# Kernel optimization log

Hardware: AMD Instinct MI355X
Metric: run time of the kernel (lower is better)

## Reference

```python
import jax, jax.numpy as jnp
import numpy as np

C = 512
NUM_HEADS = 8
HEAD_DIM = C // NUM_HEADS


def setup_inputs() -> dict:
    key = jax.random.key(0)
    ks = jax.random.split(key, 9)
    s = 1.0 / np.sqrt(C)
    x = jax.random.normal(ks[0], (8, C, 32, 32), dtype=jnp.float32)
    Wq = jax.random.uniform(ks[1], (C, C), jnp.float32, -s, s)
    bq = jax.random.uniform(ks[2], (C,), jnp.float32, -s, s)
    Wk = jax.random.uniform(ks[3], (C, C), jnp.float32, -s, s)
    bk = jax.random.uniform(ks[4], (C,), jnp.float32, -s, s)
    Wv = jax.random.uniform(ks[5], (C, C), jnp.float32, -s, s)
    bv = jax.random.uniform(ks[6], (C,), jnp.float32, -s, s)
    Wo = jax.random.uniform(ks[7], (C, C), jnp.float32, -s, s)
    bo = jax.random.uniform(ks[8], (C,), jnp.float32, -s, s)
    return {"x": x, "Wq": Wq, "bq": bq, "Wk": Wk, "bk": bk,
            "Wv": Wv, "bv": bv, "Wo": Wo, "bo": bo}


def reference(x, Wq, bq, Wk, bk, Wv, bv, Wo, bo):
    N, Cc, H, W = x.shape
    S = H * W
    # [N, S, C] token sequence
    xs = x.reshape(N, Cc, S).transpose(0, 2, 1)
    # torch Linear: y = x @ W^T + b
    q = xs @ Wq.T + bq
    k = xs @ Wk.T + bk
    v = xs @ Wv.T + bv
    # [N, h, S, d]
    q = q.reshape(N, S, NUM_HEADS, HEAD_DIM).transpose(0, 2, 1, 3)
    k = k.reshape(N, S, NUM_HEADS, HEAD_DIM).transpose(0, 2, 1, 3)
    v = v.reshape(N, S, NUM_HEADS, HEAD_DIM).transpose(0, 2, 1, 3)
    energy = jnp.einsum('nhqd,nhkd->nhqk', q, k)
    attn = jax.nn.softmax(energy / np.sqrt(HEAD_DIM), axis=3)
    out = jnp.einsum('nhql,nhld->nhqd', attn, v)
    # back to [N, S, C]; note torch reshape from (N,h,S,d) order
    out = out.reshape(N, Cc, S) if False else out.reshape(N, -1, Cc)
    out = out @ Wo.T + bo
    return out.reshape(N, Cc, H, W)


if __name__ == "__main__":
    o = reference(**setup_inputs())
    print(o.shape)
```

## Files before the change

### kernel.cpp

```cpp
#include <hip/hip_runtime.h>


typedef _Float16 f16x8 __attribute__((ext_vector_type(8)));
typedef _Float16 f16x4 __attribute__((ext_vector_type(4)));
typedef float f32x4 __attribute__((ext_vector_type(4)));

__device__ inline void gl_lds16(const void* g, void* l) {
  __builtin_amdgcn_global_load_lds((const __attribute__((address_space(1))) void*)g,
                                   (__attribute__((address_space(3))) void*)l, 16, 0, 0);
}

__device__ inline float fexp2(float x) {
#if __has_builtin(__builtin_amdgcn_exp2f)
  return __builtin_amdgcn_exp2f(x);
#else
  return exp2f(x);
#endif
}

__global__ void prep(const float* __restrict__ x,
                     const float* __restrict__ Wq, const float* __restrict__ bq,
                     const float* __restrict__ Wk, const float* __restrict__ bk,
                     const float* __restrict__ Wv, const float* __restrict__ bv,
                     const float* __restrict__ Wo,
                     _Float16* __restrict__ xs16, _Float16* __restrict__ Wqkv16,
                     float* __restrict__ bqkv, _Float16* __restrict__ Wo16) {
  __shared__ float t[32][33];
  const int tid = threadIdx.x;
  if (blockIdx.x < 1024) {
    const float g = 0.18033688011112042f;
    int i = blockIdx.x * 256 + tid;
    Wqkv16[i]          = (_Float16)(Wq[i] * g);
    Wqkv16[262144 + i] = (_Float16)Wk[i];
    Wqkv16[524288 + i] = (_Float16)Wv[i];
    Wo16[i]            = (_Float16)Wo[i];
    if (i < 512) {
      bqkv[i]        = bq[i] * g;
      bqkv[512 + i]  = bk[i];
      bqkv[1024 + i] = bv[i];
    }
    return;
  }
  const int bid = blockIdx.x - 1024;
  const int n = bid >> 9, c0 = ((bid >> 5) & 15) * 32, s0 = (bid & 31) * 32;
  const int tx = tid & 31, ty = tid >> 5;
#pragma unroll
  for (int i = 0; i < 4; ++i) {
    int cc = ty + i * 8;
    t[cc][tx] = x[((size_t)n * 512 + c0 + cc) * 1024 + s0 + tx];
  }
  __syncthreads();
#pragma unroll
  for (int i = 0; i < 4; ++i) {
    int ss = ty + i * 8;
    xs16[((size_t)n * 1024 + s0 + ss) * 512 + c0 + tx] = (_Float16)t[tx][ss];
  }
}

__global__ __launch_bounds__(256, 2) void qkv_gemm(
    const _Float16* __restrict__ A, const _Float16* __restrict__ Bw,
    const float* __restrict__ bias, _Float16* __restrict__ QK,
    _Float16* __restrict__ Vt) {
  __shared__ _Float16 smem[16896];
  _Float16* As = smem;
  _Float16* Bs = smem + 8192;
  const int tid = threadIdx.x;
  const int lane = tid & 63, w = tid >> 6;
  const int quad = lane >> 4, l15 = lane & 15;
  const int bm = blockIdx.x * 128, bn = blockIdx.y * 128;
  const int wr = (w >> 1) * 64, wc = (w & 1) * 64;
  f32x4 acc[4][4] = {};
  for (int k0 = 0; k0 < 512; k0 += 64) {
    __syncthreads();
#pragma unroll
    for (int c = 0; c < 4; ++c) {
      int idx = c * 256 + tid;
      int row = idx >> 3, sc = idx & 7;
      int kg = sc ^ (row & 7);
      gl_lds16(A + (size_t)(bm + row) * 512 + k0 + kg * 8, As + idx * 8);
      gl_lds16(Bw + (size_t)(bn + row) * 512 + k0 + kg * 8, Bs + idx * 8);
    }
    __syncthreads();
#pragma unroll
    for (int kh = 0; kh < 2; ++kh) {
      f16x8 af[4], bf[4];
#pragma unroll
      for (int i = 0; i < 4; ++i) {
        int ra = wr + i * 16 + l15;
        af[i] = *(const f16x8*)(As + ra * 64 + ((kh * 4 + quad) ^ (ra & 7)) * 8);
        int rb = wc + i * 16 + l15;
        bf[i] = *(const f16x8*)(Bs + rb * 64 + ((kh * 4 + quad) ^ (rb & 7)) * 8);
      }
#pragma unroll
      for (int i = 0; i < 4; ++i)
#pragma unroll
        for (int j = 0; j < 4; ++j)
          acc[i][j] = __builtin_amdgcn_mfma_f32_16x16x32_f16(af[i], bf[j], acc[i][j], 0, 0, 0);
    }
  }
  if (blockIdx.y < 8) {
#pragma unroll
    for (int j = 0; j < 4; ++j) {
      int col = bn + wc + j * 16 + l15;
      float bb = bias[col];
#pragma unroll
      for (int i = 0; i < 4; ++i) {
        int rowb = bm + wr + i * 16 + quad * 4;
#pragma unroll
        for (int r = 0; r < 4; ++r)
          QK[(size_t)(rowb + r) * 1024 + col] = (_Float16)(acc[i][j][r] + bb);
      }
    }
  } else {
    __syncthreads();
#pragma unroll
    for (int j = 0; j < 4; ++j) {
      int cl = wc + j * 16 + l15;
      float bb = bias[bn + cl];
#pragma unroll
      for (int i = 0; i < 4; ++i) {
        int row = wr + i * 16 + quad * 4;
        f16x4 pk;
#pragma unroll
        for (int r = 0; r < 4; ++r) pk[r] = (_Float16)(acc[i][j][r] + bb);
        *(f16x4*)(smem + cl * 132 + row) = pk;
      }
    }
    __syncthreads();
    const int n = bm >> 10, s0g = bm & 1023;
    const int vh = (bn - 1024) >> 6;
    const int cl = tid >> 1, par = tid & 1;
    const int hh = vh + (cl >> 6), d = cl & 63;
    const size_t vrow = (((size_t)((n * 8 + hh) * 64 + d)) << 10) + s0g;
#pragma unroll
    for (int g = 0; g < 8; ++g) {
      int pb = g * 16 + par * 8;
      int a32 = pb & ~31, q = (pb >> 3) & 3;
      f16x4 lo = *(const f16x4*)(smem + cl * 132 + a32 + 4 * q);
      f16x4 hi = *(const f16x4*)(smem + cl * 132 + a32 + 16 + 4 * q);
      f16x8 o = {lo[0], lo[1], lo[2], lo[3], hi[0], hi[1], hi[2], hi[3]};
      *(f16x8*)(Vt + vrow + pb) = o;
    }
  }
}

__global__ __launch_bounds__(256, 2) void attn(
    const _Float16* __restrict__ QK, const _Float16* __restrict__ Vt,
    _Float16* __restrict__ O16) {
  __shared__ _Float16 Qs[128 * 64];
  __shared__ _Float16 Ks[128 * 64];
  __shared__ _Float16 Vs[64 * 128];
  const int tid = threadIdx.x, lane = tid & 63, w = tid >> 6;
  const int quad = lane >> 4, l15 = lane & 15;
  const int n = blockIdx.y >> 3, h = blockIdx.y & 7;
  const int q0 = blockIdx.x * 128;
#pragma unroll
  for (int c = 0; c < 4; ++c) {
    int idx = c * 256 + tid;
    int row = idx >> 3, sc = idx & 7;
    int dg = sc ^ (row & 7);
    gl_lds16(QK + (size_t)(n * 1024 + q0 + row) * 1024 + h * 64 + dg * 8, Qs + idx * 8);
  }
  __syncthreads();
  f16x8 qf[2][2];
#pragma unroll
  for (int mt = 0; mt < 2; ++mt)
#pragma unroll
    for (int dc = 0; dc < 2; ++dc) {
      int row = w * 32 + mt * 16 + l15;
      qf[mt][dc] = *(const f16x8*)(Qs + row * 64 + ((dc * 4 + quad) ^ (row & 7)) * 8);
    }
  f32x4 oaccT[4][2] = {};
  f32x4 lsum[2] = {};
  const f16x8 ones = {(_Float16)1, (_Float16)1, (_Float16)1, (_Float16)1,
                      (_Float16)1, (_Float16)1, (_Float16)1, (_Float16)1};

  for (int kt = 0; kt < 8; ++kt) {
    __syncthreads();
#pragma unroll
    for (int c = 0; c < 4; ++c) {
      int idx = c * 256 + tid;
      int row = idx >> 3, sck = idx & 7;
      int dg = sck ^ (row & 7);
      gl_lds16(QK + (size_t)(n * 1024 + kt * 128 + row) * 1024 + 512 + h * 64 + dg * 8,
               Ks + idx * 8);
      int d = idx >> 4, scv = idx & 15;
      int vg = scv ^ (d & 7);
      gl_lds16(Vt + (size_t)((n * 8 + h) * 64 + d) * 1024 + kt * 128 + vg * 8,
               Vs + idx * 8);
    }
    __syncthreads();
#pragma unroll
    for (int sc = 0; sc < 4; ++sc) {
      f32x4 sacc[2][2] = {};
#pragma unroll
      for (int t = 0; t < 2; ++t) {
        int rk = (sc * 2 + t) * 16 + l15;
        f16x8 kf0 = *(const f16x8*)(Ks + rk * 64 + ((quad) ^ (rk & 7)) * 8);
        f16x8 kf1 = *(const f16x8*)(Ks + rk * 64 + ((4 + quad) ^ (rk & 7)) * 8);
#pragma unroll
        for (int mt = 0; mt < 2; ++mt) {
          sacc[mt][t] = __builtin_amdgcn_mfma_f32_16x16x32_f16(kf0, qf[mt][0], sacc[mt][t], 0, 0, 0);
          sacc[mt][t] = __builtin_amdgcn_mfma_f32_16x16x32_f16(kf1, qf[mt][1], sacc[mt][t], 0, 0, 0);
        }
      }
      f16x8 pf[2];
#pragma unroll
      for (int mt = 0; mt < 2; ++mt) {
#pragma unroll
        for (int t = 0; t < 2; ++t)
#pragma unroll
          for (int r = 0; r < 4; ++r)
            pf[mt][t * 4 + r] = (_Float16)fexp2(sacc[mt][t][r]);
        lsum[mt] = __builtin_amdgcn_mfma_f32_16x16x32_f16(pf[mt], ones, lsum[mt], 0, 0, 0);
      }
#pragma unroll
      for (int nt = 0; nt < 4; ++nt) {
        int rd = nt * 16 + l15;
        f16x8 vf = *(const f16x8*)(Vs + rd * 128 + ((sc * 4 + quad) ^ (rd & 7)) * 8);
#pragma unroll
        for (int mt = 0; mt < 2; ++mt)
          oaccT[nt][mt] = __builtin_amdgcn_mfma_f32_16x16x32_f16(vf, pf[mt], oaccT[nt][mt], 0, 0, 0);
      }
    }
  }
#pragma unroll
  for (int mt = 0; mt < 2; ++mt) {
    int r3 = l15 & 3;
    float lv = lsum[mt][0];
    lv = (r3 == 1) ? lsum[mt][1] : lv;
    lv = (r3 == 2) ? lsum[mt][2] : lv;
    lv = (r3 == 3) ? lsum[mt][3] : lv;
    float lq = __shfl(lv, (l15 >> 2) * 16 + (l15 & 3), 64);
    float rinv = 1.0f / lq;
    int q = q0 + w * 32 + mt * 16 + l15;
    int i = h * 128 + (q >> 3);
    size_t base = (size_t)(n * 1024 + i) * 512 + (q & 7) * 64 + quad * 4;
#pragma unroll
    for (int nt = 0; nt < 4; ++nt) {
      f16x4 pk;
#pragma unroll
      for (int r = 0; r < 4; ++r) pk[r] = (_Float16)(oaccT[nt][mt][r] * rinv);
      *(f16x4*)(O16 + base + nt * 16) = pk;
    }
  }
}

__global__ __launch_bounds__(256, 2) void out_gemm(
    const _Float16* __restrict__ A, const _Float16* __restrict__ Bw,
    const float* __restrict__ bias, float* __restrict__ out) {
  __shared__ _Float16 As[128 * 32];
  __shared__ _Float16 Bs[128 * 32];
  const int tid = threadIdx.x;
  const int lane = tid & 63, w = tid >> 6;
  const int quad = lane >> 4, l15 = lane & 15;
  const int bm = blockIdx.x * 128, bn = blockIdx.y * 128;
  const int wr = (w >> 1) * 64, wc = (w & 1) * 64;
  f32x4 acc[4][4] = {};
  for (int k0 = 0; k0 < 512; k0 += 32) {
    __syncthreads();
#pragma unroll
    for (int c = 0; c < 2; ++c) {
      int idx = c * 256 + tid;
      int row = idx >> 2, sc = idx & 3;
      int kg = sc ^ ((row >> 1) & 3);
      gl_lds16(A + (size_t)(bm + row) * 512 + k0 + kg * 8, As + idx * 8);
      gl_lds16(Bw + (size_t)(bn + row) * 512 + k0 + kg * 8, Bs + idx * 8);
    }
    __syncthreads();
    f16x8 af[4], bf[4];
#pragma unroll
    for (int i = 0; i < 4; ++i) {
      int ra = wr + i * 16 + l15;
      af[i] = *(const f16x8*)(As + ra * 32 + (quad ^ ((ra >> 1) & 3)) * 8);
      int rb = wc + i * 16 + l15;
      bf[i] = *(const f16x8*)(Bs + rb * 32 + (quad ^ ((rb >> 1) & 3)) * 8);
    }
#pragma unroll
    for (int i = 0; i < 4; ++i)
#pragma unroll
      for (int j = 0; j < 4; ++j)
        acc[i][j] = __builtin_amdgcn_mfma_f32_16x16x32_f16(af[i], bf[j], acc[i][j], 0, 0, 0);
  }
#pragma unroll
  for (int j = 0; j < 4; ++j) {
    int col = bn + wc + j * 16 + l15;
    float bb = bias[col];
#pragma unroll
    for (int i = 0; i < 4; ++i) {
      int rowb = bm + wr + i * 16 + quad * 4;
#pragma unroll
      for (int r = 0; r < 4; ++r)
        out[(size_t)(rowb + r) * 512 + col] = acc[i][j][r] + bb;
    }
  }
}

extern "C" void kernel_launch(void* const* d_in, const int* in_sizes, int n_in,
                              void* d_out, int out_size, void* d_ws, size_t ws_size,
                              hipStream_t stream) {
  const float* x  = (const float*)d_in[0];
  const float* Wq = (const float*)d_in[1];
  const float* bq = (const float*)d_in[2];
  const float* Wk = (const float*)d_in[3];
  const float* bk = (const float*)d_in[4];
  const float* Wv = (const float*)d_in[5];
  const float* bv = (const float*)d_in[6];
  const float* Wo = (const float*)d_in[7];
  const float* bo = (const float*)d_in[8];
  float* out = (float*)d_out;
  char* ws = (char*)d_ws;

  _Float16* xs16   = (_Float16*)(ws);
  _Float16* QK     = (_Float16*)(ws + (8u << 20));
  _Float16* Vt     = (_Float16*)(ws + (24u << 20));
  _Float16* Wqkv16 = (_Float16*)(ws + (32u << 20));
  _Float16* Wo16   = (_Float16*)(ws + (32u << 20) + 1572864);
  float*    bqkv   = (float*)   (ws + (32u << 20) + 2097152);

  hipLaunchKernelGGL(prep, dim3(5120), dim3(256), 0, stream,
                     x, Wq, bq, Wk, bk, Wv, bv, Wo, xs16, Wqkv16, bqkv, Wo16);
  hipLaunchKernelGGL(qkv_gemm, dim3(64, 12), dim3(256), 0, stream,
                     xs16, Wqkv16, bqkv, QK, Vt);
  hipLaunchKernelGGL(attn, dim3(8, 64), dim3(256), 0, stream, QK, Vt, xs16);
  hipLaunchKernelGGL(out_gemm, dim3(64, 4), dim3(256), 0, stream,
                     xs16, Wo16, bo, out);
}
```

Before: 142.3 us.

## Fuse all four stages into one persistent kernel with grid barriers

Merges the prep, QKV GEMM, attention and output GEMM kernels into a single persistent kernel of 512 blocks, with atomic-counter grid barriers between stages. This removes three kernel launch boundaries and their drain and launch gaps, at the cost of a memset plus spin-wait barriers. It relies on all 512 blocks being co-resident (2 per CU via launch bounds); otherwise it could deadlock. Some stages now leave blocks idle, such as the output GEMM using only 256 blocks and the QKV GEMM looping over 768 tiles.

```diff
diff --git a/kernel.cpp b/kernel.cpp
--- a/kernel.cpp
+++ b/kernel.cpp
@@ -18,78 +18,274 @@
 #endif
 }
 
-__global__ void prep(const float* __restrict__ x,
-                     const float* __restrict__ Wq, const float* __restrict__ bq,
-                     const float* __restrict__ Wk, const float* __restrict__ bk,
-                     const float* __restrict__ Wv, const float* __restrict__ bv,
-                     const float* __restrict__ Wo,
-                     _Float16* __restrict__ xs16, _Float16* __restrict__ Wqkv16,
-                     float* __restrict__ bqkv, _Float16* __restrict__ Wo16) {
-  __shared__ float t[32][33];
+__device__ inline void gbar(unsigned* cnt, unsigned target) {
+  __syncthreads();
+  if (threadIdx.x == 0) {
+    __threadfence();
+    atomicAdd(cnt, 1u);
+    while (atomicAdd(cnt, 0u) < target) __builtin_amdgcn_s_sleep(8);
+    __threadfence();
+  }
+  __syncthreads();
+}
+
+__global__ __launch_bounds__(256, 2) void msa_fused(
+    const float* __restrict__ x,
+    const float* __restrict__ Wq, const float* __restrict__ bq,
+    const float* __restrict__ Wk, const float* __restrict__ bk,
+    const float* __restrict__ Wv, const float* __restrict__ bv,
+    const float* __restrict__ Wo, const float* __restrict__ bo,
+    float* __restrict__ out,
+    _Float16* __restrict__ xs16, _Float16* __restrict__ Wqkv16,
+    float* __restrict__ bqkv, _Float16* __restrict__ Wo16,
+    _Float16* __restrict__ QK, _Float16* __restrict__ Vt,
+    unsigned* __restrict__ bar) {
+  __shared__ __align__(16) char smem_raw[49152];
   const int tid = threadIdx.x;
-  if (blockIdx.x < 1024) {
+  const int bid = blockIdx.x;
+  const int lane = tid & 63, wv4 = tid >> 6;
+  const int quad = lane >> 4, l15 = lane & 15;
+
+  {
     const float g = 0.18033688011112042f;
-    int i = blockIdx.x * 256 + tid;
-    Wqkv16[i]          = (_Float16)(Wq[i] * g);
-    Wqkv16[262144 + i] = (_Float16)Wk[i];
-    Wqkv16[524288 + i] = (_Float16)Wv[i];
-    Wo16[i]            = (_Float16)Wo[i];
-    if (i < 512) {
-      bqkv[i]        = bq[i] * g;
-      bqkv[512 + i]  = bk[i];
-      bqkv[1024 + i] = bv[i];
-    }
-    return;
-  }
-  const int bid = blockIdx.x - 1024;
-  const int n = bid >> 9, c0 = ((bid >> 5) & 15) * 32, s0 = (bid & 31) * 32;
-  const int tx = tid & 31, ty = tid >> 5;
-#pragma unroll
-  for (int i = 0; i < 4; ++i) {
-    int cc = ty + i * 8;
-    t[cc][tx] = x[((size_t)n * 512 + c0 + cc) * 1024 + s0 + tx];
-  }
-  __syncthreads();
-#pragma unroll
-  for (int i = 0; i < 4; ++i) {
-    int ss = ty + i * 8;
-    xs16[((size_t)n * 1024 + s0 + ss) * 512 + c0 + tx] = (_Float16)t[tx][ss];
-  }
-}
-
-__global__ __launch_bounds__(256, 2) void qkv_gemm(
-    const _Float16* __restrict__ A, const _Float16* __restrict__ Bw,
-    const float* __restrict__ bias, _Float16* __restrict__ QK,
-    _Float16* __restrict__ Vt) {
-  __shared__ _Float16 smem[16896];
-  _Float16* As = smem;
-  _Float16* Bs = smem + 8192;
-  const int tid = threadIdx.x;
-  const int lane = tid & 63, w = tid >> 6;
-  const int quad = lane >> 4, l15 = lane & 15;
-  const int bm = blockIdx.x * 128, bn = blockIdx.y * 128;
-  const int wr = (w >> 1) * 64, wc = (w & 1) * 64;
-  f32x4 acc[4][4] = {};
-  for (int k0 = 0; k0 < 512; k0 += 64) {
+#pragma unroll
+    for (int p = 0; p < 2; ++p) {
+      int i = (bid + p * 512) * 256 + tid;
+      Wqkv16[i]          = (_Float16)(Wq[i] * g);
+      Wqkv16[262144 + i] = (_Float16)Wk[i];
+      Wqkv16[524288 + i] = (_Float16)Wv[i];
+      Wo16[i]            = (_Float16)Wo[i];
+      if (i < 512) {
+        bqkv[i]        = bq[i] * g;
+        bqkv[512 + i]  = bk[i];
+        bqkv[1024 + i] = bv[i];
+      }
+    }
+    float (*t)[33] = (float (*)[33])smem_raw;
+    const int tx = tid & 31, ty = tid >> 5;
+    for (int u = bid; u < 4096; u += 512) {
+      int n = u >> 9, c0 = ((u >> 5) & 15) * 32, s0 = (u & 31) * 32;
+      __syncthreads();
+#pragma unroll
+      for (int i = 0; i < 4; ++i) {
+        int cc = ty + i * 8;
+        t[cc][tx] = x[((size_t)n * 512 + c0 + cc) * 1024 + s0 + tx];
+      }
+      __syncthreads();
+#pragma unroll
+      for (int i = 0; i < 4; ++i) {
+        int ss = ty + i * 8;
+        xs16[((size_t)n * 1024 + s0 + ss) * 512 + c0 + tx] = (_Float16)t[tx][ss];
+      }
+    }
+  }
+  gbar(bar + 0, 512);
+
+  for (int u = bid; u < 768; u += 512) {
+    _Float16* smem = (_Float16*)smem_raw;
+    _Float16* As = smem;
+    _Float16* Bs = smem + 8192;
+    const int bm = (u & 63) * 128, bn = (u >> 6) * 128;
+    const int wr = (wv4 >> 1) * 64, wc = (wv4 & 1) * 64;
+    f32x4 acc[4][4] = {};
+    for (int k0 = 0; k0 < 512; k0 += 64) {
+      __syncthreads();
+#pragma unroll
+      for (int c = 0; c < 4; ++c) {
+        int idx = c * 256 + tid;
+        int row = idx >> 3, sc = idx & 7;
+        int kg = sc ^ (row & 7);
+        gl_lds16(xs16 + (size_t)(bm + row) * 512 + k0 + kg * 8, As + idx * 8);
+        gl_lds16(Wqkv16 + (size_t)(bn + row) * 512 + k0 + kg * 8, Bs + idx * 8);
+      }
+      __syncthreads();
+#pragma unroll
+      for (int kh = 0; kh < 2; ++kh) {
+        f16x8 af[4], bf[4];
+#pragma unroll
+        for (int i = 0; i < 4; ++i) {
+          int ra = wr + i * 16 + l15;
+          af[i] = *(const f16x8*)(As + ra * 64 + ((kh * 4 + quad) ^ (ra & 7)) * 8);
+          int rb = wc + i * 16 + l15;
+          bf[i] = *(const f16x8*)(Bs + rb * 64 + ((kh * 4 + quad) ^ (rb & 7)) * 8);
+        }
+#pragma unroll
+        for (int i = 0; i < 4; ++i)
+#pragma unroll
+          for (int j = 0; j < 4; ++j)
+            acc[i][j] = __builtin_amdgcn_mfma_f32_16x16x32_f16(af[i], bf[j], acc[i][j], 0, 0, 0);
+      }
+    }
+    if ((u >> 6) < 8) {
+#pragma unroll
+      for (int j = 0; j < 4; ++j) {
+        int col = bn + wc + j * 16 + l15;
+        float bb = bqkv[col];
+#pragma unroll
+        for (int i = 0; i < 4; ++i) {
+          int rowb = bm + wr + i * 16 + quad * 4;
+#pragma unroll
+          for (int r = 0; r < 4; ++r)
+            QK[(size_t)(rowb + r) * 1024 + col] = (_Float16)(acc[i][j][r] + bb);
+        }
+      }
+    } else {
+      __syncthreads();
+#pragma unroll
+      for (int j = 0; j < 4; ++j) {
+        int cl = wc + j * 16 + l15;
+        float bb = bqkv[bn + cl];
+#pragma unroll
+        for (int i = 0; i < 4; ++i) {
+          int row = wr + i * 16 + quad * 4;
+          f16x4 pk;
+#pragma unroll
+          for (int r = 0; r < 4; ++r) pk[r] = (_Float16)(acc[i][j][r] + bb);
+          *(f16x4*)(smem + cl * 132 + row) = pk;
+        }
+      }
+      __syncthreads();
+      const int n = bm >> 10, s0g = bm & 1023;
+      const int vh = (bn - 1024) >> 6;
+      const int cl = tid >> 1, par = tid & 1;
+      const int hh = vh + (cl >> 6), d = cl & 63;
+      const size_t vrow = (((size_t)((n * 8 + hh) * 64 + d)) << 10) + s0g;
+#pragma unroll
+      for (int gq = 0; gq < 8; ++gq) {
+        int pb = gq * 16 + par * 8;
+        int a32 = pb & ~31, q = (pb >> 3) & 3;
+        f16x4 lo = *(const f16x4*)(smem + cl * 132 + a32 + 4 * q);
+        f16x4 hi = *(const f16x4*)(smem + cl * 132 + a32 + 16 + 4 * q);
+        f16x8 o = {lo[0], lo[1], lo[2], lo[3], hi[0], hi[1], hi[2], hi[3]};
+        *(f16x8*)(Vt + vrow + pb) = o;
+      }
+    }
+  }
+  gbar(bar + 1, 512);
+
+  {
+    _Float16* Qs = (_Float16*)smem_raw;
+    _Float16* Ks = Qs + 8192;
+    _Float16* Vs = Qs + 16384;
+    const int n = (bid >> 3) >> 3, h = (bid >> 3) & 7;
+    const int q0 = (bid & 7) * 128;
     __syncthreads();
 #pragma unroll
     for (int c = 0; c < 4; ++c) {
       int idx = c * 256 + tid;
       int row = idx >> 3, sc = idx & 7;
-      int kg = sc ^ (row & 7);
-      gl_lds16(A + (size_t)(bm + row) * 512 + k0 + kg * 8, As + idx * 8);
-      gl_lds16(Bw + (size_t)(bn + row) * 512 + k0 + kg * 8, Bs + idx * 8);
+      int dg = sc ^ (row & 7);
+      gl_lds16(QK + (size_t)(n * 1024 + q0 + row) * 1024 + h * 64 + dg * 8, Qs + idx * 8);
     }
     __syncthreads();
-#pragma unroll
-    for (int kh = 0; kh < 2; ++kh) {
+    f16x8 qf[2][2];
+#pragma unroll
+    for (int mt = 0; mt < 2; ++mt)
+#pragma unroll
+      for (int dc = 0; dc < 2; ++dc) {
+        int row = wv4 * 32 + mt * 16 + l15;
+        qf[mt][dc] = *(const f16x8*)(Qs + row * 64 + ((dc * 4 + quad) ^ (row & 7)) * 8);
+      }
+    f32x4 oaccT[4][2] = {};
+    f32x4 lsum[2] = {};
+    const f16x8 ones = {(_Float16)1, (_Float16)1, (_Float16)1, (_Float16)1,
+                        (_Float16)1, (_Float16)1, (_Float16)1, (_Float16)1};
+    for (int kt = 0; kt < 8; ++kt) {
+      __syncthreads();
+#pragma unroll
+      for (int c = 0; c < 4; ++c) {
+        int idx = c * 256 + tid;
+        int row = idx >> 3, sck = idx & 7;
+        int dg = sck ^ (row & 7);
+        gl_lds16(QK + (size_t)(n * 1024 + kt * 128 + row) * 1024 + 512 + h * 64 + dg * 8,
+                 Ks + idx * 8);
+        int d = idx >> 4, scv = idx & 15;
+        int vg = scv ^ (d & 7);
+        gl_lds16(Vt + (size_t)((n * 8 + h) * 64 + d) * 1024 + kt * 128 + vg * 8,
+                 Vs + idx * 8);
+      }
+      __syncthreads();
+#pragma unroll
+      for (int sc = 0; sc < 4; ++sc) {
+        f32x4 sacc[2][2] = {};
+#pragma unroll
+        for (int t = 0; t < 2; ++t) {
+          int rk = (sc * 2 + t) * 16 + l15;
+          f16x8 kf0 = *(const f16x8*)(Ks + rk * 64 + ((quad) ^ (rk & 7)) * 8);
+          f16x8 kf1 = *(const f16x8*)(Ks + rk * 64 + ((4 + quad) ^ (rk & 7)) * 8);
+#pragma unroll
+          for (int mt = 0; mt < 2; ++mt) {
+            sacc[mt][t] = __builtin_amdgcn_mfma_f32_16x16x32_f16(kf0, qf[mt][0], sacc[mt][t], 0, 0, 0);
+            sacc[mt][t] = __builtin_amdgcn_mfma_f32_16x16x32_f16(kf1, qf[mt][1], sacc[mt][t], 0, 0, 0);
+          }
+        }
+        f16x8 pf[2];
+#pragma unroll
+        for (int mt = 0; mt < 2; ++mt) {
+#pragma unroll
+          for (int t = 0; t < 2; ++t)
+#pragma unroll
+            for (int r = 0; r < 4; ++r)
+              pf[mt][t * 4 + r] = (_Float16)fexp2(sacc[mt][t][r]);
+          lsum[mt] = __builtin_amdgcn_mfma_f32_16x16x32_f16(pf[mt], ones, lsum[mt], 0, 0, 0);
+        }
+#pragma unroll
+        for (int nt = 0; nt < 4; ++nt) {
+          int rd = nt * 16 + l15;
+          f16x8 vf = *(const f16x8*)(Vs + rd * 128 + ((sc * 4 + quad) ^ (rd & 7)) * 8);
+#pragma unroll
+          for (int mt = 0; mt < 2; ++mt)
+            oaccT[nt][mt] = __builtin_amdgcn_mfma_f32_16x16x32_f16(vf, pf[mt], oaccT[nt][mt], 0, 0, 0);
+        }
+      }
+    }
+#pragma unroll
+    for (int mt = 0; mt < 2; ++mt) {
+      int r3 = l15 & 3;
+      float lv = lsum[mt][0];
+      lv = (r3 == 1) ? lsum[mt][1] : lv;
+      lv = (r3 == 2) ? lsum[mt][2] : lv;
+      lv = (r3 == 3) ? lsum[mt][3] : lv;
+      float lq = __shfl(lv, (l15 >> 2) * 16 + (l15 & 3), 64);
+      float rinv = 1.0f / lq;
+      int q = q0 + wv4 * 32 + mt * 16 + l15;
+      int i = h * 128 + (q >> 3);
+      size_t base = (size_t)(n * 1024 + i) * 512 + (q & 7) * 64 + quad * 4;
+#pragma unroll
+      for (int nt = 0; nt < 4; ++nt) {
+        f16x4 pk;
+#pragma unroll
+        for (int r = 0; r < 4; ++r) pk[r] = (_Float16)(oaccT[nt][mt][r] * rinv);
+        *(f16x4*)(xs16 + base + nt * 16) = pk;
+      }
+    }
+  }
+  gbar(bar + 2, 512);
+
+  if (bid < 256) {
+    _Float16* As = (_Float16*)smem_raw;
+    _Float16* Bs = As + 4096;
+    const int bm = (bid & 63) * 128, bn = (bid >> 6) * 128;
+    const int wr = (wv4 >> 1) * 64, wc = (wv4 & 1) * 64;
+    f32x4 acc[4][4] = {};
+    for (int k0 = 0; k0 < 512; k0 += 32) {
+      __syncthreads();
+#pragma unroll
+      for (int c = 0; c < 2; ++c) {
+        int idx = c * 256 + tid;
+        int row = idx >> 2, sc = idx & 3;
+        int kg = sc ^ ((row >> 1) & 3);
+        gl_lds16(xs16 + (size_t)(bm + row) * 512 + k0 + kg * 8, As + idx * 8);
+        gl_lds16(Wo16 + (size_t)(bn + row) * 512 + k0 + kg * 8, Bs + idx * 8);
+      }
+      __syncthreads();
       f16x8 af[4], bf[4];
 #pragma unroll
       for (int i = 0; i < 4; ++i) {
         int ra = wr + i * 16 + l15;
-        af[i] = *(const f16x8*)(As + ra * 64 + ((kh * 4 + quad) ^ (ra & 7)) * 8);
+        af[i] = *(const f16x8*)(As + ra * 32 + (quad ^ ((ra >> 1) & 3)) * 8);
         int rb = wc + i * 16 + l15;
-        bf[i] = *(const f16x8*)(Bs + rb * 64 + ((kh * 4 + quad) ^ (rb & 7)) * 8);
+        bf[i] = *(const f16x8*)(Bs + rb * 32 + (quad ^ ((rb >> 1) & 3)) * 8);
       }
 #pragma unroll
       for (int i = 0; i < 4; ++i)
@@ -97,201 +293,17 @@
         for (int j = 0; j < 4; ++j)
           acc[i][j] = __builtin_amdgcn_mfma_f32_16x16x32_f16(af[i], bf[j], acc[i][j], 0, 0, 0);
     }
-  }
-  if (blockIdx.y < 8) {
 #pragma unroll
     for (int j = 0; j < 4; ++j) {
       int col = bn + wc + j * 16 + l15;
-      float bb = bias[col];
+      float bb = bo[col];
 #pragma unroll
       for (int i = 0; i < 4; ++i) {
         int rowb = bm + wr + i * 16 + quad * 4;
 #pragma unroll
         for (int r = 0; r < 4; ++r)
-          QK[(size_t)(rowb + r) * 1024 + col] = (_Float16)(acc[i][j][r] + bb);
-      }
-    }
-  } else {
-    __syncthreads();
-#pragma unroll
-    for (int j = 0; j < 4; ++j) {
-      int cl = wc + j * 16 + l15;
-      float bb = bias[bn + cl];
-#pragma unroll
-      for (int i = 0; i < 4; ++i) {
-        int row = wr + i * 16 + quad * 4;
-        f16x4 pk;
-#pragma unroll
-        for (int r = 0; r < 4; ++r) pk[r] = (_Float16)(acc[i][j][r] + bb);
-        *(f16x4*)(smem + cl * 132 + row) = pk;
-      }
-    }
-    __syncthreads();
-    const int n = bm >> 10, s0g = bm & 1023;
-    const int vh = (bn - 1024) >> 6;
-    const int cl = tid >> 1, par = tid & 1;
-    const int hh = vh + (cl >> 6), d = cl & 63;
-    const size_t vrow = (((size_t)((n * 8 + hh) * 64 + d)) << 10) + s0g;
-#pragma unroll
-    for (int g = 0; g < 8; ++g) {
-      int pb = g * 16 + par * 8;
-      int a32 = pb & ~31, q = (pb >> 3) & 3;
-      f16x4 lo = *(const f16x4*)(smem + cl * 132 + a32 + 4 * q);
-      f16x4 hi = *(const f16x4*)(smem + cl * 132 + a32 + 16 + 4 * q);
-      f16x8 o = {lo[0], lo[1], lo[2], lo[3], hi[0], hi[1], hi[2], hi[3]};
-      *(f16x8*)(Vt + vrow + pb) = o;
-    }
-  }
-}
-
-__global__ __launch_bounds__(256, 2) void attn(
-    const _Float16* __restrict__ QK, const _Float16* __restrict__ Vt,
-    _Float16* __restrict__ O16) {
-  __shared__ _Float16 Qs[128 * 64];
-  __shared__ _Float16 Ks[128 * 64];
-  __shared__ _Float16 Vs[64 * 128];
-  const int tid = threadIdx.x, lane = tid & 63, w = tid >> 6;
-  const int quad = lane >> 4, l15 = lane & 15;
-  const int n = blockIdx.y >> 3, h = blockIdx.y & 7;
-  const int q0 = blockIdx.x * 128;
-#pragma unroll
-  for (int c = 0; c < 4; ++c) {
-    int idx = c * 256 + tid;
-    int row = idx >> 3, sc = idx & 7;
-    int dg = sc ^ (row & 7);
-    gl_lds16(QK + (size_t)(n * 1024 + q0 + row) * 1024 + h * 64 + dg * 8, Qs + idx * 8);
-  }
-  __syncthreads();
-  f16x8 qf[2][2];
-#pragma unroll
-  for (int mt = 0; mt < 2; ++mt)
-#pragma unroll
-    for (int dc = 0; dc < 2; ++dc) {
-      int row = w * 32 + mt * 16 + l15;
-      qf[mt][dc] = *(const f16x8*)(Qs + row * 64 + ((dc * 4 + quad) ^ (row & 7)) * 8);
-    }
-  f32x4 oaccT[4][2] = {};
-  f32x4 lsum[2] = {};
-  const f16x8 ones = {(_Float16)1, (_Float16)1, (_Float16)1, (_Float16)1,
-                      (_Float16)1, (_Float16)1, (_Float16)1, (_Float16)1};
-
-  for (int kt = 0; kt < 8; ++kt) {
-    __syncthreads();
-#pragma unroll
-    for (int c = 0; c < 4; ++c) {
-      int idx = c * 256 + tid;
-      int row = idx >> 3, sck = idx & 7;
-      int dg = sck ^ (row & 7);
-      gl_lds16(QK + (size_t)(n * 1024 + kt * 128 + row) * 1024 + 512 + h * 64 + dg * 8,
-               Ks + idx * 8);
-      int d = idx >> 4, scv = idx & 15;
-      int vg = scv ^ (d & 7);
-      gl_lds16(Vt + (size_t)((n * 8 + h) * 64 + d) * 1024 + kt * 128 + vg * 8,
-               Vs + idx * 8);
-    }
-    __syncthreads();
-#pragma unroll
-    for (int sc = 0; sc < 4; ++sc) {
-      f32x4 sacc[2][2] = {};
-#pragma unroll
-      for (int t = 0; t < 2; ++t) {
-        int rk = (sc * 2 + t) * 16 + l15;
-        f16x8 kf0 = *(const f16x8*)(Ks + rk * 64 + ((quad) ^ (rk & 7)) * 8);
-        f16x8 kf1 = *(const f16x8*)(Ks + rk * 64 + ((4 + quad) ^ (rk & 7)) * 8);
-#pragma unroll
-        for (int mt = 0; mt < 2; ++mt) {
-          sacc[mt][t] = __builtin_amdgcn_mfma_f32_16x16x32_f16(kf0, qf[mt][0], sacc[mt][t], 0, 0, 0);
-          sacc[mt][t] = __builtin_amdgcn_mfma_f32_16x16x32_f16(kf1, qf[mt][1], sacc[mt][t], 0, 0, 0);
-        }
-      }
-      f16x8 pf[2];
-#pragma unroll
-      for (int mt = 0; mt < 2; ++mt) {
-#pragma unroll
-        for (int t = 0; t < 2; ++t)
-#pragma unroll
-          for (int r = 0; r < 4; ++r)
-            pf[mt][t * 4 + r] = (_Float16)fexp2(sacc[mt][t][r]);
-        lsum[mt] = __builtin_amdgcn_mfma_f32_16x16x32_f16(pf[mt], ones, lsum[mt], 0, 0, 0);
-      }
-#pragma unroll
-      for (int nt = 0; nt < 4; ++nt) {
-        int rd = nt * 16 + l15;
-        f16x8 vf = *(const f16x8*)(Vs + rd * 128 + ((sc * 4 + quad) ^ (rd & 7)) * 8);
-#pragma unroll
-        for (int mt = 0; mt < 2; ++mt)
-          oaccT[nt][mt] = __builtin_amdgcn_mfma_f32_16x16x32_f16(vf, pf[mt], oaccT[nt][mt], 0, 0, 0);
-      }
-    }
-  }
-#pragma unroll
-  for (int mt = 0; mt < 2; ++mt) {
-    int r3 = l15 & 3;
-    float lv = lsum[mt][0];
-    lv = (r3 == 1) ? lsum[mt][1] : lv;
-    lv = (r3 == 2) ? lsum[mt][2] : lv;
-    lv = (r3 == 3) ? lsum[mt][3] : lv;
-    float lq = __shfl(lv, (l15 >> 2) * 16 + (l15 & 3), 64);
-    float rinv = 1.0f / lq;
-    int q = q0 + w * 32 + mt * 16 + l15;
-    int i = h * 128 + (q >> 3);
-    size_t base = (size_t)(n * 1024 + i) * 512 + (q & 7) * 64 + quad * 4;
-#pragma unroll
-    for (int nt = 0; nt < 4; ++nt) {
-      f16x4 pk;
-#pragma unroll
-      for (int r = 0; r < 4; ++r) pk[r] = (_Float16)(oaccT[nt][mt][r] * rinv);
-      *(f16x4*)(O16 + base + nt * 16) = pk;
-    }
-  }
-}
-
-__global__ __launch_bounds__(256, 2) void out_gemm(
-    const _Float16* __restrict__ A, const _Float16* __restrict__ Bw,
-    const float* __restrict__ bias, float* __restrict__ out) {
-  __shared__ _Float16 As[128 * 32];
-  __shared__ _Float16 Bs[128 * 32];
-  const int tid = threadIdx.x;
-  const int lane = tid & 63, w = tid >> 6;
-  const int quad = lane >> 4, l15 = lane & 15;
-  const int bm = blockIdx.x * 128, bn = blockIdx.y * 128;
-  const int wr = (w >> 1) * 64, wc = (w & 1) * 64;
-  f32x4 acc[4][4] = {};
-  for (int k0 = 0; k0 < 512; k0 += 32) {
-    __syncthreads();
-#pragma unroll
-    for (int c = 0; c < 2; ++c) {
-      int idx = c * 256 + tid;
-      int row = idx >> 2, sc = idx & 3;
-      int kg = sc ^ ((row >> 1) & 3);
-      gl_lds16(A + (size_t)(bm + row) * 512 + k0 + kg * 8, As + idx * 8);
-      gl_lds16(Bw + (size_t)(bn + row) * 512 + k0 + kg * 8, Bs + idx * 8);
-    }
-    __syncthreads();
-    f16x8 af[4], bf[4];
-#pragma unroll
-    for (int i = 0; i < 4; ++i) {
-      int ra = wr + i * 16 + l15;
-      af[i] = *(const f16x8*)(As + ra * 32 + (quad ^ ((ra >> 1) & 3)) * 8);
-      int rb = wc + i * 16 + l15;
-      bf[i] = *(const f16x8*)(Bs + rb * 32 + (quad ^ ((rb >> 1) & 3)) * 8);
-    }
-#pragma unroll
-    for (int i = 0; i < 4; ++i)
-#pragma unroll
-      for (int j = 0; j < 4; ++j)
-        acc[i][j] = __builtin_amdgcn_mfma_f32_16x16x32_f16(af[i], bf[j], acc[i][j], 0, 0, 0);
-  }
-#pragma unroll
-  for (int j = 0; j < 4; ++j) {
-    int col = bn + wc + j * 16 + l15;
-    float bb = bias[col];
-#pragma unroll
-    for (int i = 0; i < 4; ++i) {
-      int rowb = bm + wr + i * 16 + quad * 4;
-#pragma unroll
-      for (int r = 0; r < 4; ++r)
-        out[(size_t)(rowb + r) * 512 + col] = acc[i][j][r] + bb;
+          out[(size_t)(rowb + r) * 512 + col] = acc[i][j][r] + bb;
+      }
     }
   }
 }
@@ -317,12 +329,10 @@
   _Float16* Wqkv16 = (_Float16*)(ws + (32u << 20));
   _Float16* Wo16   = (_Float16*)(ws + (32u << 20) + 1572864);
   float*    bqkv   = (float*)   (ws + (32u << 20) + 2097152);
-
-  hipLaunchKernelGGL(prep, dim3(5120), dim3(256), 0, stream,
-                     x, Wq, bq, Wk, bk, Wv, bv, Wo, xs16, Wqkv16, bqkv, Wo16);
-  hipLaunchKernelGGL(qkv_gemm, dim3(64, 12), dim3(256), 0, stream,
-                     xs16, Wqkv16, bqkv, QK, Vt);
-  hipLaunchKernelGGL(attn, dim3(8, 64), dim3(256), 0, stream, QK, Vt, xs16);
-  hipLaunchKernelGGL(out_gemm, dim3(64, 4), dim3(256), 0, stream,
-                     xs16, Wo16, bo, out);
-}
+  unsigned* bar    = (unsigned*)(ws + (36u << 20));
+
+  hipMemsetAsync(bar, 0, 256, stream);
+  hipLaunchKernelGGL(msa_fused, dim3(512), dim3(256), 0, stream,
+                     x, Wq, bq, Wk, bk, Wv, bv, Wo, bo, out,
+                     xs16, Wqkv16, bqkv, Wo16, QK, Vt, bar);
+}
```

New measurement: 298.9 us. +110.1%, slower.
